# Kernel optimization log

Measured on AMD Instinct MI355X. Metric: run time of the kernel, lower is better.

## Reference

```python
import jax, jax.numpy as jnp
import numpy as np

X = Y = 512   # x_width = y_width
B = 8         # batch (<= bsize)
C = 32        # hidden_dim / num_feats
N_WARP = 3    # warp hidden layers
N_REND = 3    # renderer hidden layers
LRELU = 0.001


def _layer_norm(x, g, b, eps=1e-5):
    mu = x.mean(-1, keepdims=True)
    var = ((x - mu) ** 2).mean(-1, keepdims=True)
    return (x - mu) * jax.lax.rsqrt(var + eps) * g + b


def _grid_sample(img, grid):
    # img: (C,H,W) shared across batch; grid: (B,Hg,Wg,2) in [-1,1] (x,y)
    # bilinear, padding_mode='zeros', align_corners=False (torch defaults)
    Cc, H, W = img.shape
    ix = ((grid[..., 0] + 1.0) * W - 1.0) * 0.5
    iy = ((grid[..., 1] + 1.0) * H - 1.0) * 0.5
    x0f = jnp.floor(ix)
    y0f = jnp.floor(iy)
    wx1 = ix - x0f
    wy1 = iy - y0f

    def gather(xf, yf):
        valid = (xf >= 0) & (xf <= W - 1) & (yf >= 0) & (yf <= H - 1)
        xi = jnp.clip(xf, 0, W - 1).astype(jnp.int32)
        yi = jnp.clip(yf, 0, H - 1).astype(jnp.int32)
        v = img[:, yi, xi]                     # (C,B,Hg,Wg)
        return jnp.where(valid[None], v, 0.0)

    g00 = gather(x0f, y0f)
    g01 = gather(x0f + 1, y0f)
    g10 = gather(x0f, y0f + 1)
    g11 = gather(x0f + 1, y0f + 1)
    out = (g00 * ((1 - wx1) * (1 - wy1))[None]
           + g01 * (wx1 * (1 - wy1))[None]
           + g10 * ((1 - wx1) * wy1)[None]
           + g11 * (wx1 * wy1)[None])          # (C,B,Hg,Wg)
    return out.transpose(1, 0, 2, 3)           # (B,C,Hg,Wg)


def setup_inputs() -> dict:
    key = jax.random.key(0)
    ks = jax.random.split(key, 10)
    t = jax.random.uniform(ks[0], (B,), minval=-0.5, maxval=0.5)
    data = 0.1 * jax.random.normal(ks[1], (X, Y, C), dtype=jnp.float32)

    # G_FeatureTensor precomputed bilinear indices/weights (ds_factor=1)
    half = 0.5 / X
    xs = np.linspace(half, 1 - half, X, dtype=np.float64)
    xv, yv = np.meshgrid(xs, xs, indexing='ij')
    xy = np.stack([yv.ravel(), xv.ravel()], 1)          # (N,2) col0=yv col1=xv
    s = xy * np.array([X, Y], dtype=np.float64)
    idx = s.astype(np.int64)
    lerp_w = jnp.asarray(s - idx, dtype=jnp.float32)    # (N,2)
    x0 = jnp.asarray(np.clip(idx[:, 0], 0, X - 1), dtype=jnp.int32)
    y0 = jnp.asarray(np.clip(idx[:, 1], 0, Y - 1), dtype=jnp.int32)
    x1 = jnp.minimum(x0 + 1, X - 1)
    y1 = jnp.minimum(y0 + 1, Y - 1)

    lin = np.linspace(-1, 1, X, dtype=np.float32)
    gx, gy = np.meshgrid(lin, lin, indexing='xy')
    xy_basis = jnp.asarray(np.stack([gx, gy], -1))      # (X,Y,2)

    def lw(k, fan_in, shape):
        return (1.0 / np.sqrt(fan_in)) * jax.random.normal(k, shape, dtype=jnp.float32)

    kw = jax.random.split(ks[2], 8)
    return {
        't': t, 'data': data, 'lerp_w': lerp_w, 'xy_basis': xy_basis,
        'w_in': lw(kw[0], 3, (3, C)), 'b_in': jnp.zeros((C,)),
        'w_h': lw(kw[1], C, (N_WARP, C, C)), 'b_h': jnp.zeros((N_WARP, C)),
        'ln_g': jnp.ones((N_WARP, C)), 'ln_b': jnp.zeros((N_WARP, C)),
        'w_out': lw(kw[2], C, (C, 2)), 'b_out': jnp.zeros((2,)),
        'r_wh': lw(kw[3], C, (N_REND, C, C)), 'r_bh': jnp.zeros((N_REND, C)),
        'r_wo': lw(kw[4], C, (C, 1)), 'r_bo': jnp.zeros((1,)),
        'x0': x0, 'y0': y0, 'x1': x1, 'y1': y1,
    }


def reference(t, data, lerp_w, xy_basis, w_in, b_in, w_h, b_h, ln_g, ln_b,
              w_out, b_out, r_wh, r_bh, r_wo, r_bo, x0, y0, x1, y1):
    Bn = t.shape[0]
    wA = lerp_w[:, 0:1]
    wB = lerp_w[:, 1:2]
    # manual 4-corner bilinear gather over the learned feature grid
    feats = (data[y0, x0] * (1 - wA) * (1 - wB)
             + data[y0, x1] * wA * (1 - wB)
             + data[y1, x0] * (1 - wA) * wB
             + data[y1, x1] * wA * wB)                  # (N,C)
    feat_img = feats.reshape(X, Y, C).transpose(2, 0, 1)  # (C,X,Y)

    alpha = (t + 0.5)[:, None]                          # (B,1)
    t_emb = jnp.broadcast_to(alpha[:, None, None, :], (Bn, X, Y, 1))
    t_in = jnp.concatenate(
        [jnp.broadcast_to(xy_basis, (Bn, X, Y, 2)), t_emb], -1)  # (B,X,Y,3)

    h = t_in @ w_in + b_in
    for i in range(N_WARP):
        h = jnp.sin(_layer_norm(h @ w_h[i] + b_h[i], ln_g[i], ln_b[i]))
    motion = (h @ w_out + b_out) * 0.1                  # (B,X,Y,2)

    grid = motion + xy_basis                             # (B,X,Y,2)
    f = _grid_sample(feat_img, grid)                     # (B,C,X,Y)

    z = f.transpose(0, 2, 3, 1)
    for i in range(N_REND):
        z = jax.nn.relu(z @ r_wh[i] + r_bh[i])
    out = (z @ r_wo + r_bo).transpose(0, 3, 1, 2)        # (B,1,X,Y)
    return jnp.where(out >= 0, out, LRELU * out)
```

## Files before the change

### kernel.cpp

```cpp
#include <hip/hip_runtime.h>

#define XDIM 512
#define CDIM 32
#define NPIX (XDIM * XDIM)
#define NB 8

typedef short bf16x8 __attribute__((ext_vector_type(8)));
typedef float f32x4 __attribute__((ext_vector_type(4)));
typedef float f32x16 __attribute__((ext_vector_type(16)));

#define FEATS_BYTES (NPIX * CDIM * 4)

__device__ __forceinline__ short f2bf(float v) {
    __bf16 b = (__bf16)v;
    return __builtin_bit_cast(short, b);
}
__device__ __forceinline__ float bfup(short s) {
    return (float)__builtin_bit_cast(__bf16, s);
}

__global__ __launch_bounds__(64) void wprep_kernel(
    const float* __restrict__ w_h, const float* __restrict__ r_wh,
    unsigned short* __restrict__ afrag)
{
    int L = blockIdx.x >> 1;
    int T = blockIdx.x & 1;
    int l = threadIdx.x;
    const float* W = (L < 3) ? (w_h + L * CDIM * CDIM) : (r_wh + (L - 3) * CDIM * CDIM);
    int m = l & 31;
    int h = l >> 5;
    unsigned short* dh = afrag + (((L * 2 + T) * 2 + 0) * 64 + l) * 8;
    unsigned short* dl = afrag + (((L * 2 + T) * 2 + 1) * 64 + l) * 8;
    for (int j = 0; j < 8; j++) {
        int c = 16 * T + 4 * h + (j & 3) + 8 * (j >> 2);
        float v = W[c * CDIM + m];
        short hi = f2bf(v);
        short lo = f2bf(v - bfup(hi));
        dh[j] = (unsigned short)hi;
        dl[j] = (unsigned short)lo;
    }
}

__global__ __launch_bounds__(256) void feats_kernel(
    const float* __restrict__ data, const float* __restrict__ lerp_w,
    const int* __restrict__ x0, const int* __restrict__ y0,
    const int* __restrict__ x1, const int* __restrict__ y1,
    float* __restrict__ feats)
{
    int tid = blockIdx.x * 256 + threadIdx.x;
    int p = tid >> 5;
    int c = tid & 31;
    if (p >= NPIX) return;
    float wA = lerp_w[p * 2 + 0];
    float wB = lerp_w[p * 2 + 1];
    int xa = x0[p], ya = y0[p], xb = x1[p], yb = y1[p];
    float v00 = data[(ya * XDIM + xa) * CDIM + c];
    float v01 = data[(ya * XDIM + xb) * CDIM + c];
    float v10 = data[(yb * XDIM + xa) * CDIM + c];
    float v11 = data[(yb * XDIM + xb) * CDIM + c];
    float r = v00 * (1.f - wA) * (1.f - wB) + v01 * wA * (1.f - wB)
            + v10 * (1.f - wA) * wB + v11 * wA * wB;
    feats[p * CDIM + c] = r;
}

__device__ __forceinline__ void build2(const float a[16], bf16x8 bh[2], bf16x8 bl[2]) {
    #pragma unroll
    for (int r = 0; r < 16; r++) {
        short hi = f2bf(a[r]);
        bh[r >> 3][r & 7] = hi;
        bl[r >> 3][r & 7] = f2bf(a[r] - bfup(hi));
    }
}

__device__ __forceinline__ f32x16 matmul6(
    const unsigned short* __restrict__ afrag, int L, int lane,
    const bf16x8 bh[2], const bf16x8 bl[2])
{
    const bf16x8* ap = (const bf16x8*)afrag;
    f32x16 acc = {0.f, 0.f, 0.f, 0.f, 0.f, 0.f, 0.f, 0.f,
                  0.f, 0.f, 0.f, 0.f, 0.f, 0.f, 0.f, 0.f};
    #pragma unroll
    for (int T = 0; T < 2; T++) {
        bf16x8 ah = ap[((L * 2 + T) * 2 + 0) * 64 + lane];
        bf16x8 al = ap[((L * 2 + T) * 2 + 1) * 64 + lane];
        acc = __builtin_amdgcn_mfma_f32_32x32x16_bf16(al, bh[T], acc, 0, 0, 0);
        acc = __builtin_amdgcn_mfma_f32_32x32x16_bf16(ah, bl[T], acc, 0, 0, 0);
        acc = __builtin_amdgcn_mfma_f32_32x32x16_bf16(ah, bh[T], acc, 0, 0, 0);
    }
    return acc;
}

__global__ __launch_bounds__(256) void fused_mfma_kernel(
    const float* __restrict__ t, const float* __restrict__ xy_basis,
    const float* __restrict__ w_in, const float* __restrict__ b_in,
    const float* __restrict__ b_h,
    const float* __restrict__ ln_g, const float* __restrict__ ln_b,
    const float* __restrict__ w_out, const float* __restrict__ b_out,
    const float* __restrict__ r_bh,
    const float* __restrict__ r_wo, const float* __restrict__ r_bo,
    const float* __restrict__ feats, const unsigned short* __restrict__ afrag,
    float* __restrict__ out)
{
    int lane = threadIdx.x & 63;
    int p = lane & 31, h = lane >> 5;

    int bid = blockIdx.x;
    int swz = (bid & 7) * 2048 + (bid >> 3);
    int gw = swz * 4 + (int)(threadIdx.x >> 6);
    int b = gw & 7;
    int pbase = (gw >> 3) << 5;
    int pix = pbase + p;

    float alpha = t[b] + 0.5f;
    float2 xy = ((const float2*)xy_basis)[pix];

    float a[16];
    #pragma unroll
    for (int g = 0; g < 4; g++) {
        int c = 8 * g + 4 * h;
        f32x4 w0 = *(const f32x4*)(w_in + c);
        f32x4 w1 = *(const f32x4*)(w_in + CDIM + c);
        f32x4 w2 = *(const f32x4*)(w_in + 2 * CDIM + c);
        f32x4 bb = *(const f32x4*)(b_in + c);
        #pragma unroll
        for (int i = 0; i < 4; i++)
            a[4 * g + i] = fmaf(xy.x, w0[i], fmaf(xy.y, w1[i], fmaf(alpha, w2[i], bb[i])));
    }

    #pragma unroll 1
    for (int L = 0; L < 3; L++) {
        bf16x8 bh[2], bl[2];
        build2(a, bh, bl);
        f32x16 acc = matmul6(afrag, L, lane, bh, bl);

        float sum = 0.f, sq = 0.f;
        #pragma unroll
        for (int g = 0; g < 4; g++) {
            f32x4 bia = *(const f32x4*)(b_h + L * CDIM + 8 * g + 4 * h);
            #pragma unroll
            for (int i = 0; i < 4; i++) {
                float v = acc[4 * g + i] + bia[i];
                a[4 * g + i] = v;
                sum += v;
                sq = fmaf(v, v, sq);
            }
        }
        sum += __shfl_xor(sum, 32, 64);
        sq  += __shfl_xor(sq, 32, 64);
        float mu = sum * (1.f / 32.f);
        float var = fmaf(sq, 1.f / 32.f, -mu * mu);
        float rs = rsqrtf(var + 1e-5f);
        #pragma unroll
        for (int g = 0; g < 4; g++) {
            f32x4 gg = *(const f32x4*)(ln_g + L * CDIM + 8 * g + 4 * h);
            f32x4 be = *(const f32x4*)(ln_b + L * CDIM + 8 * g + 4 * h);
            #pragma unroll
            for (int i = 0; i < 4; i++)
                a[4 * g + i] = __sinf(fmaf((a[4 * g + i] - mu) * rs, gg[i], be[i]));
        }
    }

    float mx = 0.f, my = 0.f;
    #pragma unroll
    for (int g = 0; g < 4; g++) {
        int c = 8 * g + 4 * h;
        f32x4 wa = *(const f32x4*)(w_out + 2 * c);
        f32x4 wb = *(const f32x4*)(w_out + 2 * c + 4);
        mx = fmaf(a[4 * g + 0], wa[0], mx); my = fmaf(a[4 * g + 0], wa[1], my);
        mx = fmaf(a[4 * g + 1], wa[2], mx); my = fmaf(a[4 * g + 1], wa[3], my);
        mx = fmaf(a[4 * g + 2], wb[0], mx); my = fmaf(a[4 * g + 2], wb[1], my);
        mx = fmaf(a[4 * g + 3], wb[2], mx); my = fmaf(a[4 * g + 3], wb[3], my);
    }
    mx += __shfl_xor(mx, 32, 64);
    my += __shfl_xor(my, 32, 64);
    float gridx = fmaf(mx + b_out[0], 0.1f, xy.x);
    float gridy = fmaf(my + b_out[1], 0.1f, xy.y);

    float ix = ((gridx + 1.0f) * (float)XDIM - 1.0f) * 0.5f;
    float iy = ((gridy + 1.0f) * (float)XDIM - 1.0f) * 0.5f;
    float x0f = floorf(ix), y0f = floorf(iy);
    float wx = ix - x0f, wy = iy - y0f;
    #pragma unroll
    for (int r = 0; r < 16; r++) a[r] = 0.f;
    #pragma unroll
    for (int corner = 0; corner < 4; corner++) {
        float xf = x0f + (float)(corner & 1);
        float yf = y0f + (float)(corner >> 1);
        float w = ((corner & 1) ? wx : 1.f - wx) * ((corner >> 1) ? wy : 1.f - wy);
        bool valid = (xf >= 0.f) && (xf <= (float)(XDIM - 1)) &&
                     (yf >= 0.f) && (yf <= (float)(XDIM - 1));
        if (!valid) w = 0.f;
        int xi = (int)fminf(fmaxf(xf, 0.f), (float)(XDIM - 1));
        int yi = (int)fminf(fmaxf(yf, 0.f), (float)(XDIM - 1));
        const float* fp = feats + (yi * XDIM + xi) * CDIM + 4 * h;
        #pragma unroll
        for (int g = 0; g < 4; g++) {
            f32x4 v = *(const f32x4*)(fp + 8 * g);
            #pragma unroll
            for (int i = 0; i < 4; i++)
                a[4 * g + i] = fmaf(w, v[i], a[4 * g + i]);
        }
    }

    #pragma unroll 1
    for (int L = 3; L < 6; L++) {
        bf16x8 bh[2], bl[2];
        build2(a, bh, bl);
        f32x16 acc = matmul6(afrag, L, lane, bh, bl);
        #pragma unroll
        for (int g = 0; g < 4; g++) {
            f32x4 bia = *(const f32x4*)(r_bh + (L - 3) * CDIM + 8 * g + 4 * h);
            #pragma unroll
            for (int i = 0; i < 4; i++)
                a[4 * g + i] = fmaxf(acc[4 * g + i] + bia[i], 0.f);
        }
    }

    float o = 0.f;
    #pragma unroll
    for (int g = 0; g < 4; g++) {
        f32x4 wz = *(const f32x4*)(r_wo + 8 * g + 4 * h);
        #pragma unroll
        for (int i = 0; i < 4; i++) o = fmaf(a[4 * g + i], wz[i], o);
    }
    o += __shfl_xor(o, 32, 64);
    o += r_bo[0];
    o = (o >= 0.f) ? o : 0.001f * o;
    if (h == 0) out[b * NPIX + pix] = o;
}

extern "C" void kernel_launch(void* const* d_in, const int* in_sizes, int n_in,
                              void* d_out, int out_size, void* d_ws, size_t ws_size,
                              hipStream_t stream) {
    const float* t        = (const float*)d_in[0];
    const float* data     = (const float*)d_in[1];
    const float* lerp_w   = (const float*)d_in[2];
    const float* xy_basis = (const float*)d_in[3];
    const float* w_in     = (const float*)d_in[4];
    const float* b_in     = (const float*)d_in[5];
    const float* w_h      = (const float*)d_in[6];
    const float* b_h      = (const float*)d_in[7];
    const float* ln_g     = (const float*)d_in[8];
    const float* ln_b     = (const float*)d_in[9];
    const float* w_out    = (const float*)d_in[10];
    const float* b_out    = (const float*)d_in[11];
    const float* r_wh     = (const float*)d_in[12];
    const float* r_bh     = (const float*)d_in[13];
    const float* r_wo     = (const float*)d_in[14];
    const float* r_bo     = (const float*)d_in[15];
    const int* x0 = (const int*)d_in[16];
    const int* y0 = (const int*)d_in[17];
    const int* x1 = (const int*)d_in[18];
    const int* y1 = (const int*)d_in[19];

    float* feats = (float*)d_ws;
    unsigned short* afrag = (unsigned short*)((char*)d_ws + FEATS_BYTES);
    float* out = (float*)d_out;

    wprep_kernel<<<12, 64, 0, stream>>>(w_h, r_wh, afrag);
    feats_kernel<<<(NPIX * CDIM) / 256, 256, 0, stream>>>(data, lerp_w, x0, y0, x1, y1, feats);
    fused_mfma_kernel<<<(NB * NPIX) / 128, 256, 0, stream>>>(
        t, xy_basis, w_in, b_in, b_h, ln_g, ln_b, w_out, b_out,
        r_bh, r_wo, r_bo, feats, afrag, out);
}
```

Measured before the change: 320.8 us.

## Prefetch MFMA weight fragments early and split accumulators across K halves

Weight fragments for each layer are now loaded into registers well before use (warp layers 0-1 at kernel start, layer 2 mid-chain, renderer layers before the grid-sample gather), so their global-load latency overlaps other work. The layer loops are fully unrolled through helper functions. Each matmul now uses two independent accumulators, one per K half, which interleaves the dependent MFMA chain and sums the halves afterwards. Launch bounds now request 4 blocks per CU. The extra live fragment registers may raise register pressure or spill under that occupancy target.

Measured after the change: 321.0 us. Within noise of the previous version (+0.1%).

```diff
diff --git a/kernel.cpp b/kernel.cpp
--- a/kernel.cpp
+++ b/kernel.cpp
@@ -72,25 +72,89 @@
     }
 }
 
-__device__ __forceinline__ f32x16 matmul6(
-    const unsigned short* __restrict__ afrag, int L, int lane,
-    const bf16x8 bh[2], const bf16x8 bl[2])
-{
-    const bf16x8* ap = (const bf16x8*)afrag;
-    f32x16 acc = {0.f, 0.f, 0.f, 0.f, 0.f, 0.f, 0.f, 0.f,
-                  0.f, 0.f, 0.f, 0.f, 0.f, 0.f, 0.f, 0.f};
-    #pragma unroll
-    for (int T = 0; T < 2; T++) {
-        bf16x8 ah = ap[((L * 2 + T) * 2 + 0) * 64 + lane];
-        bf16x8 al = ap[((L * 2 + T) * 2 + 1) * 64 + lane];
-        acc = __builtin_amdgcn_mfma_f32_32x32x16_bf16(al, bh[T], acc, 0, 0, 0);
-        acc = __builtin_amdgcn_mfma_f32_32x32x16_bf16(ah, bl[T], acc, 0, 0, 0);
-        acc = __builtin_amdgcn_mfma_f32_32x32x16_bf16(ah, bh[T], acc, 0, 0, 0);
-    }
-    return acc;
-}
-
-__global__ __launch_bounds__(256) void fused_mfma_kernel(
+__device__ __forceinline__ void matmul_split(
+    const bf16x8 fh[2], const bf16x8 fl[2],
+    const bf16x8 bh[2], const bf16x8 bl[2],
+    f32x16& accA, f32x16& accB)
+{
+    f32x16 z = {0.f, 0.f, 0.f, 0.f, 0.f, 0.f, 0.f, 0.f,
+                0.f, 0.f, 0.f, 0.f, 0.f, 0.f, 0.f, 0.f};
+    accA = z; accB = z;
+    accA = __builtin_amdgcn_mfma_f32_32x32x16_bf16(fl[0], bh[0], accA, 0, 0, 0);
+    accB = __builtin_amdgcn_mfma_f32_32x32x16_bf16(fl[1], bh[1], accB, 0, 0, 0);
+    accA = __builtin_amdgcn_mfma_f32_32x32x16_bf16(fh[0], bl[0], accA, 0, 0, 0);
+    accB = __builtin_amdgcn_mfma_f32_32x32x16_bf16(fh[1], bl[1], accB, 0, 0, 0);
+    accA = __builtin_amdgcn_mfma_f32_32x32x16_bf16(fh[0], bh[0], accA, 0, 0, 0);
+    accB = __builtin_amdgcn_mfma_f32_32x32x16_bf16(fh[1], bh[1], accB, 0, 0, 0);
+}
+
+__device__ __forceinline__ void warp_layer(
+    float a[16], const bf16x8 fh[2], const bf16x8 fl[2],
+    const float* __restrict__ bias, const float* __restrict__ gamma,
+    const float* __restrict__ beta, int h)
+{
+    bf16x8 bh[2], bl[2];
+    build2(a, bh, bl);
+    f32x16 accA, accB;
+    matmul_split(fh, fl, bh, bl, accA, accB);
+
+    float sum = 0.f, sq = 0.f;
+    #pragma unroll
+    for (int g = 0; g < 4; g++) {
+        f32x4 bia = *(const f32x4*)(bias + 8 * g + 4 * h);
+        #pragma unroll
+        for (int i = 0; i < 4; i++) {
+            int r = 4 * g + i;
+            float v = (accA[r] + accB[r]) + bia[i];
+            a[r] = v;
+            sum += v;
+            sq = fmaf(v, v, sq);
+        }
+    }
+    sum += __shfl_xor(sum, 32, 64);
+    sq  += __shfl_xor(sq, 32, 64);
+    float mu = sum * (1.f / 32.f);
+    float var = fmaf(sq, 1.f / 32.f, -mu * mu);
+    float rs = rsqrtf(var + 1e-5f);
+    #pragma unroll
+    for (int g = 0; g < 4; g++) {
+        f32x4 gg = *(const f32x4*)(gamma + 8 * g + 4 * h);
+        f32x4 be = *(const f32x4*)(beta + 8 * g + 4 * h);
+        #pragma unroll
+        for (int i = 0; i < 4; i++) {
+            int r = 4 * g + i;
+            a[r] = __sinf(fmaf((a[r] - mu) * rs, gg[i], be[i]));
+        }
+    }
+}
+
+__device__ __forceinline__ void render_layer(
+    float a[16], const bf16x8 fh[2], const bf16x8 fl[2],
+    const float* __restrict__ bias, int h)
+{
+    bf16x8 bh[2], bl[2];
+    build2(a, bh, bl);
+    f32x16 accA, accB;
+    matmul_split(fh, fl, bh, bl, accA, accB);
+    #pragma unroll
+    for (int g = 0; g < 4; g++) {
+        f32x4 bia = *(const f32x4*)(bias + 8 * g + 4 * h);
+        #pragma unroll
+        for (int i = 0; i < 4; i++) {
+            int r = 4 * g + i;
+            a[r] = fmaxf((accA[r] + accB[r]) + bia[i], 0.f);
+        }
+    }
+}
+
+#define LOADFRAG(L, FH, FL) do { \
+    FH[0] = ap[(((L) * 2 + 0) * 2 + 0) * 64 + lane]; \
+    FL[0] = ap[(((L) * 2 + 0) * 2 + 1) * 64 + lane]; \
+    FH[1] = ap[(((L) * 2 + 1) * 2 + 0) * 64 + lane]; \
+    FL[1] = ap[(((L) * 2 + 1) * 2 + 1) * 64 + lane]; \
+} while (0)
+
+__global__ __launch_bounds__(256, 4) void fused_mfma_kernel(
     const float* __restrict__ t, const float* __restrict__ xy_basis,
     const float* __restrict__ w_in, const float* __restrict__ b_in,
     const float* __restrict__ b_h,
@@ -111,6 +175,12 @@
     int pbase = (gw >> 3) << 5;
     int pix = pbase + p;
 
+    const bf16x8* ap = (const bf16x8*)afrag;
+
+    bf16x8 fAh[2], fAl[2], fBh[2], fBl[2], fCh[2], fCl[2];
+    LOADFRAG(0, fAh, fAl);
+    LOADFRAG(1, fBh, fBl);
+
     float alpha = t[b] + 0.5f;
     float2 xy = ((const float2*)xy_basis)[pix];
 
@@ -127,38 +197,10 @@
             a[4 * g + i] = fmaf(xy.x, w0[i], fmaf(xy.y, w1[i], fmaf(alpha, w2[i], bb[i])));
     }
 
-    #pragma unroll 1
-    for (int L = 0; L < 3; L++) {
-        bf16x8 bh[2], bl[2];
-        build2(a, bh, bl);
-        f32x16 acc = matmul6(afrag, L, lane, bh, bl);
-
-        float sum = 0.f, sq = 0.f;
-        #pragma unroll
-        for (int g = 0; g < 4; g++) {
-            f32x4 bia = *(const f32x4*)(b_h + L * CDIM + 8 * g + 4 * h);
-            #pragma unroll
-            for (int i = 0; i < 4; i++) {
-                float v = acc[4 * g + i] + bia[i];
-                a[4 * g + i] = v;
-                sum += v;
-                sq = fmaf(v, v, sq);
-            }
-        }
-        sum += __shfl_xor(sum, 32, 64);
-        sq  += __shfl_xor(sq, 32, 64);
-        float mu = sum * (1.f / 32.f);
-        float var = fmaf(sq, 1.f / 32.f, -mu * mu);
-        float rs = rsqrtf(var + 1e-5f);
-        #pragma unroll
-        for (int g = 0; g < 4; g++) {
-            f32x4 gg = *(const f32x4*)(ln_g + L * CDIM + 8 * g + 4 * h);
-            f32x4 be = *(const f32x4*)(ln_b + L * CDIM + 8 * g + 4 * h);
-            #pragma unroll
-            for (int i = 0; i < 4; i++)
-                a[4 * g + i] = __sinf(fmaf((a[4 * g + i] - mu) * rs, gg[i], be[i]));
-        }
-    }
+    warp_layer(a, fAh, fAl, b_h + 0 * CDIM, ln_g + 0 * CDIM, ln_b + 0 * CDIM, h);
+    LOADFRAG(2, fCh, fCl);
+    warp_layer(a, fBh, fBl, b_h + 1 * CDIM, ln_g + 1 * CDIM, ln_b + 1 * CDIM, h);
+    warp_layer(a, fCh, fCl, b_h + 2 * CDIM, ln_g + 2 * CDIM, ln_b + 2 * CDIM, h);
 
     float mx = 0.f, my = 0.f;
     #pragma unroll
@@ -175,6 +217,11 @@
     my += __shfl_xor(my, 32, 64);
     float gridx = fmaf(mx + b_out[0], 0.1f, xy.x);
     float gridy = fmaf(my + b_out[1], 0.1f, xy.y);
+
+    bf16x8 r0h[2], r0l[2], r1h[2], r1l[2], r2h[2], r2l[2];
+    LOADFRAG(3, r0h, r0l);
+    LOADFRAG(4, r1h, r1l);
+    LOADFRAG(5, r2h, r2l);
 
     float ix = ((gridx + 1.0f) * (float)XDIM - 1.0f) * 0.5f;
     float iy = ((gridy + 1.0f) * (float)XDIM - 1.0f) * 0.5f;
@@ -202,19 +249,9 @@
         }
     }
 
-    #pragma unroll 1
-    for (int L = 3; L < 6; L++) {
-        bf16x8 bh[2], bl[2];
-        build2(a, bh, bl);
-        f32x16 acc = matmul6(afrag, L, lane, bh, bl);
-        #pragma unroll
-        for (int g = 0; g < 4; g++) {
-            f32x4 bia = *(const f32x4*)(r_bh + (L - 3) * CDIM + 8 * g + 4 * h);
-            #pragma unroll
-            for (int i = 0; i < 4; i++)
-                a[4 * g + i] = fmaxf(acc[4 * g + i] + bia[i], 0.f);
-        }
-    }
+    render_layer(a, r0h, r0l, r_bh + 0 * CDIM, h);
+    render_layer(a, r1h, r1l, r_bh + 1 * CDIM, h);
+    render_layer(a, r2h, r2l, r_bh + 2 * CDIM, h);
 
     float o = 0.f;
     #pragma unroll
```
